# Kernel tuning notes

Hardware: AMD Instinct MI355X
Metric: run time of the kernel (lower is better)

The kernel has to match this reference:

```python
import jax, jax.numpy as jnp
import numpy as np

NUM_GRAPHS = 64
HID = 6
NUM_CLASSES = 10
NUM_FEATS = 128


def setup_inputs() -> dict:
    key = jax.random.key(0)
    ks = jax.random.split(key, 20)
    N, E = 100000, 3200000
    x = jax.random.normal(ks[0], (N, NUM_FEATS), dtype=jnp.float32)
    edge_index = jax.random.randint(ks[1], (2, E), 0, N, dtype=jnp.int64)
    batch = jnp.sort(jax.random.randint(ks[2], (N,), 0, NUM_GRAPHS, dtype=jnp.int64))
    def glorot(k, fan_in, fan_out):
        lim = np.sqrt(6.0 / (fan_in + fan_out))
        return jax.random.uniform(k, (fan_in, fan_out), jnp.float32, -lim, lim)
    inp = {"x": x, "edge_index": edge_index, "batch": batch}
    dims = [(NUM_FEATS, HID)] + [(HID, HID)] * 5 + [(HID, NUM_CLASSES)]
    names = ["1", "2", "3", "4", "5", "6", "f"]
    for i, (nm, (fi, fo)) in enumerate(zip(names, dims)):
        inp["W" + nm] = glorot(ks[3 + i], fi, fo)
        inp["b" + nm] = jnp.zeros((fo,), jnp.float32)
    return inp


def _gcn_forward(x, edge_index, batch, Ws, bs):
    N = x.shape[0]
    loop = jnp.arange(N, dtype=edge_index.dtype)
    src = jnp.concatenate([edge_index[0], loop])  # self-loops appended
    dst = jnp.concatenate([edge_index[1], loop])
    deg = jax.ops.segment_sum(jnp.ones_like(dst, dtype=x.dtype), dst, num_segments=N)
    dinv = jnp.where(deg > 0, jax.lax.rsqrt(deg), 0.0)
    norm = dinv[src] * dinv[dst]  # [E+N]

    def conv(h, W, b):
        h = h @ W  # [N, out]
        agg = jax.ops.segment_sum(h[src] * norm[:, None], dst, num_segments=N)
        return agg + b

    h = x
    for W, b in zip(Ws, bs):
        h = jax.nn.relu(conv(h, W, b))

    # global mean pool over graphs
    sums = jax.ops.segment_sum(h, batch, num_segments=NUM_GRAPHS)
    cnts = jax.ops.segment_sum(jnp.ones((N,), h.dtype), batch, num_segments=NUM_GRAPHS)
    pooled = sums / jnp.maximum(cnts, 1.0)[:, None]
    return jax.nn.log_softmax(pooled, axis=1)


def reference(x, edge_index, batch, W1, b1, W2, b2, W3, b3, W4, b4, W5, b5, W6, b6, Wf, bf):
    Ws = [W1, W2, W3, W4, W5, W6, Wf]
    bs = [b1, b2, b3, b4, b5, b6, bf]
    return _gcn_forward(x, edge_index, batch, Ws, bs)
```

## Files before the change

### kernel.cpp

```cpp
#include <hip/hip_runtime.h>
#include <hip/hip_bf16.h>
#include <hip/hip_fp16.h>
#include <math.h>

#define NF     128
#define HID    6
#define NC     10
#define NG     64
#define SLOTS  64
#define OVFCAP 8192

#define BKT_SH    7
#define BKT_NODES 128
#define NBK_MAX   1024
#define EPB       4096
#define BCAP      5120
#define BOVFCAP   4096

__device__ __forceinline__ void addh(float* a, uint4 q) {
    const __half2* h = (const __half2*)&q;
    float2 f0 = __half22float2(h[0]);
    float2 f1 = __half22float2(h[1]);
    float2 f2 = __half22float2(h[2]);
    a[0] += f0.x; a[1] += f0.y; a[2] += f1.x;
    a[3] += f1.y; a[4] += f2.x; a[5] += f2.y;
}

__device__ __forceinline__ uint4 packh(const float* v) {
    uint4 q;
    __half2* h = (__half2*)&q;
    h[0] = __floats2half2_rn(v[0], v[1]);
    h[1] = __floats2half2_rn(v[2], v[3]);
    h[2] = __floats2half2_rn(v[4], v[5]);
    h[3] = __floats2half2_rn(0.f, 0.f);
    return q;
}

__global__ __launch_bounds__(256) void bucket_scatter_kernel(
        const int* __restrict__ src, const int* __restrict__ dst, int E, int nbk,
        int* __restrict__ bucket_cursor, unsigned int* __restrict__ bucket_arr,
        int* __restrict__ bovf_meta, int2* __restrict__ bovf) {
    __shared__ int cntL[NBK_MAX];
    __shared__ int offs[NBK_MAX + 1];
    __shared__ int gb[NBK_MAX];
    __shared__ int wtot[4];
    __shared__ unsigned int stage[EPB];
    int tid = threadIdx.x;
    for (int k = tid; k < NBK_MAX; k += 256) cntL[k] = 0;
    __syncthreads();
    int e0 = blockIdx.x * EPB;
    int cnt_e = E - e0; if (cnt_e > EPB) cnt_e = EPB;
    int sreg[16], dreg[16], rank[16];
    if (cnt_e == EPB && (E & 3) == 0) {
        const int4* s4p = (const int4*)(src + e0);
        const int4* d4p = (const int4*)(dst + e0);
#pragma unroll
        for (int k = 0; k < 4; ++k) {
            int4 sv = s4p[k * 256 + tid];
            int4 dv = d4p[k * 256 + tid];
            sreg[4*k+0] = sv.x; sreg[4*k+1] = sv.y; sreg[4*k+2] = sv.z; sreg[4*k+3] = sv.w;
            dreg[4*k+0] = dv.x; dreg[4*k+1] = dv.y; dreg[4*k+2] = dv.z; dreg[4*k+3] = dv.w;
        }
#pragma unroll
        for (int k = 0; k < 16; ++k) rank[k] = atomicAdd(&cntL[dreg[k] >> BKT_SH], 1);
    } else {
#pragma unroll
        for (int k = 0; k < 16; ++k) {
            int e = e0 + k * 256 + tid;
            if (e < E) {
                dreg[k] = dst[e]; sreg[k] = src[e];
                rank[k] = atomicAdd(&cntL[dreg[k] >> BKT_SH], 1);
            } else dreg[k] = -1;
        }
    }
    __syncthreads();
    int base = tid * 4;
    int c0 = cntL[base], c1 = cntL[base + 1], c2 = cntL[base + 2], c3 = cntL[base + 3];
    int tsum = c0 + c1 + c2 + c3;
    int lane = tid & 63, wv = tid >> 6;
    int v = tsum;
#pragma unroll
    for (int off = 1; off < 64; off <<= 1) {
        int u = __shfl_up(v, off);
        if (lane >= off) v += u;
    }
    if (lane == 63) wtot[wv] = v;
    __syncthreads();
    int wbase = 0;
    for (int w = 0; w < wv; ++w) wbase += wtot[w];
    int ex = wbase + v - tsum;
    offs[base]     = ex;
    offs[base + 1] = ex + c0;
    offs[base + 2] = ex + c0 + c1;
    offs[base + 3] = ex + c0 + c1 + c2;
    if (tid == 0) offs[NBK_MAX] = cnt_e;
    for (int bb = tid; bb < nbk; bb += 256) {
        int c = cntL[bb];
        if (c > 0) gb[bb] = atomicAdd(&bucket_cursor[bb], c);
    }
    __syncthreads();
#pragma unroll
    for (int k = 0; k < 16; ++k) {
        int d = dreg[k];
        if (d < 0) continue;
        int b = d >> BKT_SH;
        stage[offs[b] + rank[k]] =
            (unsigned int)(d & (BKT_NODES - 1)) | ((unsigned int)sreg[k] << BKT_SH);
    }
    __syncthreads();
    for (int j = tid; j < cnt_e; j += 256) {
        unsigned int p = stage[j];
        int lo = 0, hi = NBK_MAX;
        while (hi - lo > 1) {
            int mid = (lo + hi) >> 1;
            if (offs[mid] <= j) lo = mid; else hi = mid;
        }
        int b = lo;
        int grel = gb[b] + (j - offs[b]);
        if (grel < BCAP) {
            bucket_arr[(size_t)b * BCAP + grel] = p;
        } else {
            int d = (b << BKT_SH) | (int)(p & (BKT_NODES - 1));
            int s = (int)(p >> BKT_SH);
            int p2 = atomicAdd(bovf_meta, 1);
            if (p2 < BOVFCAP) bovf[p2] = make_int2(d, s);
        }
    }
}

__global__ __launch_bounds__(256) void ell_build_kernel(
        const unsigned int* __restrict__ bucket_arr, const int* __restrict__ bucket_cursor,
        const int* __restrict__ bovf_meta, const int2* __restrict__ bovf,
        int* __restrict__ ell, int* __restrict__ cnt, float* __restrict__ dinv,
        int* __restrict__ ovf_meta, int* __restrict__ ovf_dst, int* __restrict__ ovf_src,
        int N) {
    __shared__ int ell_s[BKT_NODES * SLOTS];
    __shared__ int cur[BKT_NODES];
    int b = blockIdx.x;
    int tid = threadIdx.x;
    if (tid < BKT_NODES) cur[tid] = 0;
    __syncthreads();
    int bc = bucket_cursor[b];
    if (bc > BCAP) bc = BCAP;
    const unsigned int* ba = bucket_arr + (size_t)b * BCAP;
    for (int j = tid; j < bc; j += 256) {
        unsigned int p = ba[j];
        int r = (int)(p & (BKT_NODES - 1));
        int s = (int)(p >> BKT_SH);
        int slot = atomicAdd(&cur[r], 1);
        if (slot < SLOTS) {
            ell_s[r * SLOTS + slot] = s;
        } else {
            int d = (b << BKT_SH) + r;
            int q = atomicAdd(ovf_meta, 1);
            if (q < OVFCAP) { ovf_dst[q] = d; ovf_src[q] = s; }
        }
    }
    int m = *bovf_meta;
    if (m > BOVFCAP) m = BOVFCAP;
    for (int t = tid; t < m; t += 256) {
        int2 e = bovf[t];
        if ((e.x >> BKT_SH) == b) {
            int r = e.x & (BKT_NODES - 1);
            int slot = atomicAdd(&cur[r], 1);
            if (slot < SLOTS) {
                ell_s[r * SLOTS + slot] = e.y;
            } else {
                int q = atomicAdd(ovf_meta, 1);
                if (q < OVFCAP) { ovf_dst[q] = e.x; ovf_src[q] = e.y; }
            }
        }
    }
    __syncthreads();
    int nid0 = b << BKT_SH;
    int rows = N - nid0; if (rows > BKT_NODES) rows = BKT_NODES;
    if (rows <= 0) return;
    int4* eg = (int4*)(ell + (size_t)nid0 * SLOTS);
    const int4* es = (const int4*)ell_s;
    for (int k = tid; k < rows * (SLOTS / 4); k += 256) {
        int r = k >> 4;
        int q = k & 15;
        int c = cur[r]; if (c > SLOTS) c = SLOTS;
        if (q * 4 < c) eg[k] = es[k];
    }
    for (int r = tid; r < rows; r += 256) {
        int deg = cur[r];
        cnt[nid0 + r] = deg;
        dinv[nid0 + r] = rsqrtf((float)deg + 1.0f);
    }
}

__global__ __launch_bounds__(256) void layer1_kernel(const float* __restrict__ x,
                                                     const float* __restrict__ W,
                                                     const float* __restrict__ dinv,
                                                     uint4* __restrict__ g16, int N) {
    __shared__ float sW[8 * 100];
    for (int idx = threadIdx.x; idx < NF * HID; idx += 256) {
        int s = idx / 96, r = idx % 96;
        int o = r / 16, j = r % 16;
        sW[s * 100 + o * 16 + j] = W[(s * 16 + j) * HID + o];
    }
    __syncthreads();
    int t = blockIdx.x * 256 + threadIdx.x;
    int i = t >> 3;
    int sub = t & 7;
    if (i >= N) return;
    const float4* xr = (const float4*)(x + (size_t)i * NF + sub * 16);
    float4 xv0 = xr[0], xv1 = xr[1], xv2 = xr[2], xv3 = xr[3];
    const float4* wr = (const float4*)(sW + sub * 100);
    float p[HID];
#pragma unroll
    for (int o = 0; o < HID; ++o) {
        float4 w0 = wr[o * 4 + 0], w1 = wr[o * 4 + 1], w2 = wr[o * 4 + 2], w3 = wr[o * 4 + 3];
        p[o] = xv0.x * w0.x + xv0.y * w0.y + xv0.z * w0.z + xv0.w * w0.w
             + xv1.x * w1.x + xv1.y * w1.y + xv1.z * w1.z + xv1.w * w1.w
             + xv2.x * w2.x + xv2.y * w2.y + xv2.z * w2.z + xv2.w * w2.w
             + xv3.x * w3.x + xv3.y * w3.y + xv3.z * w3.z + xv3.w * w3.w;
    }
#pragma unroll
    for (int m = 1; m < 8; m <<= 1) {
#pragma unroll
        for (int o = 0; o < HID; ++o) p[o] += __shfl_xor(p[o], m);
    }
    if (sub == 0) {
        float dv = dinv[i];
        float v[HID];
#pragma unroll
        for (int o = 0; o < HID; ++o) v[o] = dv * p[o];
        g16[i] = packh(v);
    }
}

__device__ __forceinline__ void gather8h(int ne, const int* __restrict__ er,
                                         const uint4* __restrict__ g16, int sub,
                                         float* acc) {
#pragma unroll
    for (int r = 0; r < SLOTS / 32; ++r) {
        int base = r * 32 + sub * 4;
        if (base < ne) {
            int4 q = *(const int4*)(er + base);
            int s0 = q.x;
            int s1 = (base + 1 < ne) ? q.y : s0;
            int s2 = (base + 2 < ne) ? q.z : s0;
            int s3 = (base + 3 < ne) ? q.w : s0;
            uint4 v0 = g16[s0];
            uint4 v1 = g16[s1];
            uint4 v2 = g16[s2];
            uint4 v3 = g16[s3];
            addh(acc, v0);
            if (base + 1 < ne) addh(acc, v1);
            if (base + 2 < ne) addh(acc, v2);
            if (base + 3 < ne) addh(acc, v3);
        }
    }
}

template<int PREP>
__global__ __launch_bounds__(256) void gcn_layer8_kernel(
        const int* __restrict__ cnt, const int* __restrict__ ell,
        const int* __restrict__ ovf_meta, const int* __restrict__ ovf_dst,
        const int* __restrict__ ovf_src, const float* __restrict__ dinv,
        const uint4* __restrict__ gin, uint4* __restrict__ gout,
        const float* __restrict__ W, const float* __restrict__ b, int N) {
    int t = blockIdx.x * 256 + threadIdx.x;
    int i = t >> 3;
    int sub = t & 7;
    if (i >= N) return;
    int n = cnt[i];
    int ne = n < SLOTS ? n : SLOTS;
    const int* er = ell + (size_t)i * SLOTS;
    float acc[HID] = {0.f, 0.f, 0.f, 0.f, 0.f, 0.f};
    gather8h(ne, er, gin, sub, acc);
    if (sub == 0) addh(acc, gin[i]);
    if (n > SLOTS && sub == 2) {
        int m = ovf_meta[0];
        m = m < OVFCAP ? m : OVFCAP;
        for (int tt = 0; tt < m; ++tt) {
            if (ovf_dst[tt] == i) addh(acc, gin[ovf_src[tt]]);
        }
    }
#pragma unroll
    for (int m = 1; m < 8; m <<= 1) {
#pragma unroll
        for (int f = 0; f < HID; ++f) acc[f] += __shfl_xor(acc[f], m);
    }
    if (sub != 0) return;
    float dv = dinv[i];
    float h[HID];
#pragma unroll
    for (int f = 0; f < HID; ++f) {
        float u = dv * acc[f] + b[f];
        h[f] = u > 0.0f ? u : 0.0f;
    }
    float o[HID];
    if (PREP) {
#pragma unroll
        for (int f = 0; f < HID; ++f) o[f] = dv * h[f];
    } else {
#pragma unroll
        for (int fo = 0; fo < HID; ++fo) {
            float s = 0.0f;
#pragma unroll
            for (int fi = 0; fi < HID; ++fi) s += h[fi] * W[fi * HID + fo];
            o[fo] = dv * s;
        }
    }
    gout[i] = packh(o);
}

__global__ __launch_bounds__(256) void pool_kernel(
        const int* __restrict__ cnt, const int* __restrict__ ell,
        const int* __restrict__ ovf_meta, const int* __restrict__ ovf_dst,
        const int* __restrict__ ovf_src, const float* __restrict__ dinv,
        const uint4* __restrict__ gin, const int* __restrict__ batch,
        const float* __restrict__ Wf, const float* __restrict__ bf,
        float* __restrict__ pooled, float* __restrict__ gcnt, int N) {
    __shared__ float sp[NG * NC];
    __shared__ float sc[NG];
    __shared__ int srange[2];
    for (int k = threadIdx.x; k < NG * NC; k += 256) sp[k] = 0.0f;
    if (threadIdx.x < NG) sc[threadIdx.x] = 0.0f;
    int start = blockIdx.x * 32;
    int endi = min(start + 32, N) - 1;
    if (threadIdx.x == 0) {
        srange[0] = batch[start];
        srange[1] = batch[endi];
    }
    __syncthreads();
    int t = blockIdx.x * 256 + threadIdx.x;
    int i = t >> 3;
    int sub = t & 7;
    if (i < N) {
        int n = cnt[i];
        int ne = n < SLOTS ? n : SLOTS;
        const int* er = ell + (size_t)i * SLOTS;
        float acc[HID] = {0.f, 0.f, 0.f, 0.f, 0.f, 0.f};
        gather8h(ne, er, gin, sub, acc);
        if (sub == 0) addh(acc, gin[i]);
        if (n > SLOTS && sub == 2) {
            int m = ovf_meta[0];
            m = m < OVFCAP ? m : OVFCAP;
            for (int tt = 0; tt < m; ++tt) {
                if (ovf_dst[tt] == i) addh(acc, gin[ovf_src[tt]]);
            }
        }
#pragma unroll
        for (int m = 1; m < 8; m <<= 1) {
#pragma unroll
            for (int f = 0; f < HID; ++f) acc[f] += __shfl_xor(acc[f], m);
        }
        if (sub == 0) {
            float dv = dinv[i];
            float u[HID];
#pragma unroll
            for (int f = 0; f < HID; ++f) u[f] = dv * acc[f];
            int bg = batch[i];
#pragma unroll
            for (int c = 0; c < NC; ++c) {
                float v = bf[c];
#pragma unroll
                for (int f = 0; f < HID; ++f) v += u[f] * Wf[f * NC + c];
                v = v > 0.0f ? v : 0.0f;
                atomicAdd(&sp[bg * NC + c], v);
            }
            atomicAdd(&sc[bg], 1.0f);
        }
    }
    __syncthreads();
    int bmin = srange[0], bmax = srange[1];
    int rows = bmax - bmin + 1;
    for (int k = threadIdx.x; k < rows * NC; k += 256) {
        int r = bmin + k / NC, c = k % NC;
        float v = sp[r * NC + c];
        if (v != 0.0f) atomicAdd(&pooled[r * NC + c], v);
    }
    for (int k = threadIdx.x; k < rows; k += 256) {
        float v = sc[bmin + k];
        if (v != 0.0f) atomicAdd(&gcnt[bmin + k], v);
    }
}

__global__ void logsm_kernel(const float* __restrict__ pooled, const float* __restrict__ gcnt,
                             float* __restrict__ out) {
    int gidx = threadIdx.x;
    if (gidx >= NG) return;
    float c = gcnt[gidx];
    c = c > 1.0f ? c : 1.0f;
    float v[NC];
    float m = -1e30f;
#pragma unroll
    for (int k = 0; k < NC; ++k) {
        v[k] = pooled[gidx * NC + k] / c;
        m = v[k] > m ? v[k] : m;
    }
    float s = 0.0f;
#pragma unroll
    for (int k = 0; k < NC; ++k) s += expf(v[k] - m);
    float ls = logf(s);
#pragma unroll
    for (int k = 0; k < NC; ++k) out[gidx * NC + k] = v[k] - m - ls;
}

extern "C" void kernel_launch(void* const* d_in, const int* in_sizes, int n_in,
                              void* d_out, int out_size, void* d_ws, size_t ws_size,
                              hipStream_t stream) {
    const float* x     = (const float*)d_in[0];
    const int*   ei    = (const int*)d_in[1];
    const int*   batch = (const int*)d_in[2];
    const float* W[7];
    const float* b[7];
    for (int l = 0; l < 7; ++l) {
        W[l] = (const float*)d_in[3 + 2 * l];
        b[l] = (const float*)d_in[4 + 2 * l];
    }
    const int N = in_sizes[2];
    const int E = in_sizes[1] / 2;
    const int nbk = (N + BKT_NODES - 1) >> BKT_SH;
    const int* src = ei;
    const int* dst = ei + E;
    float* out = (float*)d_out;

    char* wp = (char*)d_ws;
    int* bucket_cursor = (int*)wp;  wp += (size_t)NBK_MAX * 4;
    int* ovf_meta  = (int*)wp;      wp += 16;
    int* bovf_meta = (int*)wp;      wp += 16;
    int* ovf_dst   = (int*)wp;      wp += OVFCAP * 4;
    int* ovf_src   = (int*)wp;      wp += OVFCAP * 4;
    int2* bovf     = (int2*)wp;     wp += (size_t)BOVFCAP * 8;
    int* cnt       = (int*)wp;      wp += (((size_t)N * 4 + 15) & ~15ull);
    float* dinv    = (float*)wp;    wp += (((size_t)N * 4 + 15) & ~15ull);
    uint4* g_a     = (uint4*)wp;    wp += (size_t)N * 16;
    uint4* g_b     = (uint4*)wp;    wp += (size_t)N * 16;
    float* pooled  = (float*)wp;    wp += NG * NC * 4;
    float* gcnt    = (float*)wp;    wp += (((size_t)NG * 4 + 15) & ~15ull);
    int* ell       = (int*)wp;      wp += (size_t)N * SLOTS * 4;
    unsigned int* bucket_arr = (unsigned int*)wp;  wp += (size_t)nbk * BCAP * 4;

    hipMemsetAsync(bucket_cursor, 0, (size_t)NBK_MAX * 4 + 32, stream);
    hipMemsetAsync(pooled, 0, (NG * NC + NG) * sizeof(float), stream);

    const int BT = 256;
    int bn8 = ((size_t)N * 8 + BT - 1) / BT;
    int bp1 = (E + EPB - 1) / EPB;

    bucket_scatter_kernel<<<bp1, BT, 0, stream>>>(src, dst, E, nbk, bucket_cursor,
                                                  bucket_arr, bovf_meta, bovf);
    ell_build_kernel<<<nbk, BT, 0, stream>>>(bucket_arr, bucket_cursor, bovf_meta, bovf,
                                             ell, cnt, dinv, ovf_meta, ovf_dst, ovf_src, N);

    layer1_kernel<<<bn8, BT, 0, stream>>>(x, W[0], dinv, g_a, N);

    gcn_layer8_kernel<0><<<bn8, BT, 0, stream>>>(cnt, ell, ovf_meta, ovf_dst, ovf_src, dinv, g_a, g_b, W[1], b[0], N);
    gcn_layer8_kernel<0><<<bn8, BT, 0, stream>>>(cnt, ell, ovf_meta, ovf_dst, ovf_src, dinv, g_b, g_a, W[2], b[1], N);
    gcn_layer8_kernel<0><<<bn8, BT, 0, stream>>>(cnt, ell, ovf_meta, ovf_dst, ovf_src, dinv, g_a, g_b, W[3], b[2], N);
    gcn_layer8_kernel<0><<<bn8, BT, 0, stream>>>(cnt, ell, ovf_meta, ovf_dst, ovf_src, dinv, g_b, g_a, W[4], b[3], N);
    gcn_layer8_kernel<0><<<bn8, BT, 0, stream>>>(cnt, ell, ovf_meta, ovf_dst, ovf_src, dinv, g_a, g_b, W[5], b[4], N);
    gcn_layer8_kernel<1><<<bn8, BT, 0, stream>>>(cnt, ell, ovf_meta, ovf_dst, ovf_src, dinv, g_b, g_a, nullptr, b[5], N);
    pool_kernel<<<bn8, BT, 0, stream>>>(cnt, ell, ovf_meta, ovf_dst, ovf_src, dinv, g_a, batch, W[6], b[6], pooled, gcnt, N);
    logsm_kernel<<<1, 64, 0, stream>>>(pooled, gcnt, out);
}
```

Baseline: 353.5 us.

## Accumulate gathers in packed half2 and pad ELL with a zero sentinel row

The neighbour gather now accumulates in packed __half2 registers and does the cross-lane shuffle reduction on packed halves, which cuts conversion and add instructions. Empty ELL slots are pre-filled with index N, and a zero row at g16[N] is written each layer, so the per-element bounds selects and branches inside the 4-wide gather disappear. In exchange, summing up to ~64 terms in fp16 loses precision and can overflow, and each feature buffer grows by one row.

```diff
diff --git a/kernel.cpp b/kernel.cpp
--- a/kernel.cpp
+++ b/kernel.cpp
@@ -17,13 +17,18 @@
 #define BCAP      5120
 #define BOVFCAP   4096
 
-__device__ __forceinline__ void addh(float* a, uint4 q) {
+__device__ __forceinline__ void addh2(__half2& a0, __half2& a1, __half2& a2, uint4 q) {
     const __half2* h = (const __half2*)&q;
-    float2 f0 = __half22float2(h[0]);
-    float2 f1 = __half22float2(h[1]);
-    float2 f2 = __half22float2(h[2]);
-    a[0] += f0.x; a[1] += f0.y; a[2] += f1.x;
-    a[3] += f1.y; a[4] += f2.x; a[5] += f2.y;
+    a0 = __hadd2(a0, h[0]);
+    a1 = __hadd2(a1, h[1]);
+    a2 = __hadd2(a2, h[2]);
+}
+
+__device__ __forceinline__ __half2 shfl_xor_h2(__half2 v, int m) {
+    union { __half2 h; unsigned int u; } a;
+    a.h = v;
+    a.u = __shfl_xor(a.u, m);
+    return a.h;
 }
 
 __device__ __forceinline__ uint4 packh(const float* v) {
@@ -139,6 +144,7 @@
     int b = blockIdx.x;
     int tid = threadIdx.x;
     if (tid < BKT_NODES) cur[tid] = 0;
+    for (int k = tid; k < BKT_NODES * SLOTS; k += 256) ell_s[k] = N;
     __syncthreads();
     int bc = bucket_cursor[b];
     if (bc > BCAP) bc = BCAP;
@@ -204,6 +210,7 @@
     int t = blockIdx.x * 256 + threadIdx.x;
     int i = t >> 3;
     int sub = t & 7;
+    if (t == 0) g16[N] = make_uint4(0u, 0u, 0u, 0u);
     if (i >= N) return;
     const float4* xr = (const float4*)(x + (size_t)i * NF + sub * 16);
     float4 xv0 = xr[0], xv1 = xr[1], xv2 = xr[2], xv3 = xr[3];
@@ -233,24 +240,20 @@
 
 __device__ __forceinline__ void gather8h(int ne, const int* __restrict__ er,
                                          const uint4* __restrict__ g16, int sub,
-                                         float* acc) {
+                                         __half2& a0, __half2& a1, __half2& a2) {
 #pragma unroll
     for (int r = 0; r < SLOTS / 32; ++r) {
         int base = r * 32 + sub * 4;
         if (base < ne) {
             int4 q = *(const int4*)(er + base);
-            int s0 = q.x;
-            int s1 = (base + 1 < ne) ? q.y : s0;
-            int s2 = (base + 2 < ne) ? q.z : s0;
-            int s3 = (base + 3 < ne) ? q.w : s0;
-            uint4 v0 = g16[s0];
-            uint4 v1 = g16[s1];
-            uint4 v2 = g16[s2];
-            uint4 v3 = g16[s3];
-            addh(acc, v0);
-            if (base + 1 < ne) addh(acc, v1);
-            if (base + 2 < ne) addh(acc, v2);
-            if (base + 3 < ne) addh(acc, v3);
+            uint4 v0 = g16[q.x];
+            uint4 v1 = g16[q.y];
+            uint4 v2 = g16[q.z];
+            uint4 v3 = g16[q.w];
+            addh2(a0, a1, a2, v0);
+            addh2(a0, a1, a2, v1);
+            addh2(a0, a1, a2, v2);
+            addh2(a0, a1, a2, v3);
         }
     }
 }
@@ -265,26 +268,30 @@
     int t = blockIdx.x * 256 + threadIdx.x;
     int i = t >> 3;
     int sub = t & 7;
+    if (t == 0) gout[N] = make_uint4(0u, 0u, 0u, 0u);
     if (i >= N) return;
     int n = cnt[i];
     int ne = n < SLOTS ? n : SLOTS;
     const int* er = ell + (size_t)i * SLOTS;
-    float acc[HID] = {0.f, 0.f, 0.f, 0.f, 0.f, 0.f};
-    gather8h(ne, er, gin, sub, acc);
-    if (sub == 0) addh(acc, gin[i]);
+    __half2 a0 = __float2half2_rn(0.f), a1 = a0, a2 = a0;
+    gather8h(ne, er, gin, sub, a0, a1, a2);
+    if (sub == 0) addh2(a0, a1, a2, gin[i]);
     if (n > SLOTS && sub == 2) {
         int m = ovf_meta[0];
         m = m < OVFCAP ? m : OVFCAP;
         for (int tt = 0; tt < m; ++tt) {
-            if (ovf_dst[tt] == i) addh(acc, gin[ovf_src[tt]]);
+            if (ovf_dst[tt] == i) addh2(a0, a1, a2, gin[ovf_src[tt]]);
         }
     }
 #pragma unroll
     for (int m = 1; m < 8; m <<= 1) {
-#pragma unroll
-        for (int f = 0; f < HID; ++f) acc[f] += __shfl_xor(acc[f], m);
+        a0 = __hadd2(a0, shfl_xor_h2(a0, m));
+        a1 = __hadd2(a1, shfl_xor_h2(a1, m));
+        a2 = __hadd2(a2, shfl_xor_h2(a2, m));
     }
     if (sub != 0) return;
+    float2 f0 = __half22float2(a0), f1 = __half22float2(a1), f2 = __half22float2(a2);
+    float acc[HID] = { f0.x, f0.y, f1.x, f1.y, f2.x, f2.y };
     float dv = dinv[i];
     float h[HID];
 #pragma unroll
@@ -334,22 +341,25 @@
         int n = cnt[i];
         int ne = n < SLOTS ? n : SLOTS;
         const int* er = ell + (size_t)i * SLOTS;
-        float acc[HID] = {0.f, 0.f, 0.f, 0.f, 0.f, 0.f};
-        gather8h(ne, er, gin, sub, acc);
-        if (sub == 0) addh(acc, gin[i]);
+        __half2 a0 = __float2half2_rn(0.f), a1 = a0, a2 = a0;
+        gather8h(ne, er, gin, sub, a0, a1, a2);
+        if (sub == 0) addh2(a0, a1, a2, gin[i]);
         if (n > SLOTS && sub == 2) {
             int m = ovf_meta[0];
             m = m < OVFCAP ? m : OVFCAP;
             for (int tt = 0; tt < m; ++tt) {
-                if (ovf_dst[tt] == i) addh(acc, gin[ovf_src[tt]]);
+                if (ovf_dst[tt] == i) addh2(a0, a1, a2, gin[ovf_src[tt]]);
             }
         }
 #pragma unroll
         for (int m = 1; m < 8; m <<= 1) {
-#pragma unroll
-            for (int f = 0; f < HID; ++f) acc[f] += __shfl_xor(acc[f], m);
+            a0 = __hadd2(a0, shfl_xor_h2(a0, m));
+            a1 = __hadd2(a1, shfl_xor_h2(a1, m));
+            a2 = __hadd2(a2, shfl_xor_h2(a2, m));
         }
         if (sub == 0) {
+            float2 f0 = __half22float2(a0), f1 = __half22float2(a1), f2 = __half22float2(a2);
+            float acc[HID] = { f0.x, f0.y, f1.x, f1.y, f2.x, f2.y };
             float dv = dinv[i];
             float u[HID];
 #pragma unroll
@@ -429,8 +439,8 @@
     int2* bovf     = (int2*)wp;     wp += (size_t)BOVFCAP * 8;
     int* cnt       = (int*)wp;      wp += (((size_t)N * 4 + 15) & ~15ull);
     float* dinv    = (float*)wp;    wp += (((size_t)N * 4 + 15) & ~15ull);
-    uint4* g_a     = (uint4*)wp;    wp += (size_t)N * 16;
-    uint4* g_b     = (uint4*)wp;    wp += (size_t)N * 16;
+    uint4* g_a     = (uint4*)wp;    wp += (size_t)(N + 1) * 16;
+    uint4* g_b     = (uint4*)wp;    wp += (size_t)(N + 1) * 16;
     float* pooled  = (float*)wp;    wp += NG * NC * 4;
     float* gcnt    = (float*)wp;    wp += (((size_t)NG * 4 + 15) & ~15ull);
     int* ell       = (int*)wp;      wp += (size_t)N * SLOTS * 4;
```

After: 345.3 us. 1.02x faster.
